# Kernel optimization log

Measured on AMD Instinct MI355X. Metric: run time of the kernel, lower is better.

## Reference

```python
import jax, jax.numpy as jnp
import numpy as np

EMBED_DIM = 1024
NUM_HEADS = 16
HEAD_DIM = EMBED_DIM // NUM_HEADS
SCALING = HEAD_DIM ** -0.5
TGT_LEN = 2048
BSZ = 2


def setup_inputs() -> dict:
    key = jax.random.key(0)
    ks = jax.random.split(key, 8)
    E = EMBED_DIM
    query = jax.random.normal(ks[0], (TGT_LEN, BSZ, E), dtype=jnp.float32)
    k_in = jax.random.normal(ks[1], (TGT_LEN, BSZ, E), dtype=jnp.float32)
    v_in = jax.random.normal(ks[2], (TGT_LEN, BSZ, E), dtype=jnp.float32)
    attn_mask = jnp.zeros((TGT_LEN, TGT_LEN), dtype=jnp.float32)
    key_padding_mask = jnp.zeros((1, TGT_LEN, TGT_LEN), dtype=jnp.int32)
    # torch.nn.Linear params: y = x @ W.T + b
    lim_qkv = 1.0 / np.sqrt(E)
    W_qkv = jax.random.uniform(ks[3], (3 * E, E), minval=-lim_qkv, maxval=lim_qkv, dtype=jnp.float32)
    b_qkv = jax.random.uniform(ks[4], (3 * E,), minval=-lim_qkv, maxval=lim_qkv, dtype=jnp.float32)
    W_out = jax.random.uniform(ks[5], (E, E), minval=-lim_qkv, maxval=lim_qkv, dtype=jnp.float32)
    b_out = jax.random.uniform(ks[6], (E,), minval=-lim_qkv, maxval=lim_qkv, dtype=jnp.float32)
    return {"query": query, "key": k_in, "value": v_in, "attn_mask": attn_mask,
            "key_padding_mask": key_padding_mask, "W_qkv": W_qkv, "b_qkv": b_qkv,
            "W_out": W_out, "b_out": b_out}


def reference(query, key, value, attn_mask, key_padding_mask, W_qkv, b_qkv, W_out, b_out):
    # NOTE: original module ignores `key`/`value` args (self-attn from query only).
    T, B, E = query.shape
    H, hd = NUM_HEADS, HEAD_DIM
    neg_inf = jnp.float32(-jnp.inf)
    qkv = query @ W_qkv.T + b_qkv                       # [T, B, 3E]
    qkv = jnp.transpose(qkv.reshape(T, B * H, 3 * hd), (1, 0, 2))  # [BH, T, 3hd]
    q, k, v = jnp.split(qkv, 3, axis=-1)                # each [BH, T, hd]
    aw = jnp.einsum('btd,bsd->bts', q, k) * SCALING     # [BH, T, T]
    # quirk of original: exact-zero scores become -inf
    aw = jnp.where(aw == 0, neg_inf, aw)
    am = jnp.where(attn_mask == 0, jnp.float32(0.0), attn_mask * jnp.float32(-10000.0))
    aw = aw + am
    aw = jnp.where(jnp.swapaxes(key_padding_mask, -2, -1) == 0, aw, neg_inf)
    aw = jax.nn.softmax(aw, axis=-1)
    # dropout p=0.0 -> identity
    out = aw @ v                                        # [BH, T, hd]
    # faithful to original: transpose(0,1) then reshape(bsz, tgt_len, E)
    out = jnp.swapaxes(out, 0, 1).reshape(B, T, E)      # [B, T, E]
    return out @ W_out.T + b_out
```

## Files before the change

### kernel.cpp

```cpp
#include <hip/hip_runtime.h>
#include <math.h>

#define TLEN 2048
#define EMB 1024
#define QKVD 3072
#define NROWS 4096
#define LOG2E 1.4426950408889634f

typedef unsigned short u16;
typedef unsigned int u32;
using frag_ab = __attribute__((ext_vector_type(8))) short;
using f32x4   = __attribute__((ext_vector_type(4))) float;

__device__ __forceinline__ u16 f2bf(float x) {
    u32 u = __builtin_bit_cast(u32, x);
    u = (u + 0x7FFFu + ((u >> 16) & 1u)) >> 16;
    return (u16)u;
}

__device__ __forceinline__ u32 cvt_pk_bf16(float lo, float hi) {
    u32 r;
    asm("v_cvt_pk_bf16_f32 %0, %1, %2" : "=v"(r) : "v"(lo), "v"(hi));
    return r;
}

__device__ __forceinline__ float exp2_hw(float x) {
    float r;
    asm("v_exp_f32 %0, %1" : "=v"(r) : "v"(x));
    return r;
}

#define GLL16(g, l) __builtin_amdgcn_global_load_lds(                         \
    (const __attribute__((address_space(1))) void*)(g),                       \
    (__attribute__((address_space(3))) void*)(l), 16, 0, 0)

__global__ __launch_bounds__(256)
void prep(const float* __restrict__ qa, const float* __restrict__ wqkv,
          const float* __restrict__ wout, u16* __restrict__ out,
          const float* __restrict__ am, const int* __restrict__ kpm,
          float* __restrict__ cm, int* __restrict__ flags)
{
    __shared__ int kt[64][65];
    __shared__ int s_any;
    const int tid = threadIdx.x;
    const int bid = blockIdx.x;
    if (bid < 4096) {
        int i = (bid * 256 + tid) * 8;
        const float* src;
        int off;
        if (i < 4194304)      { src = qa;   off = i; }
        else if (i < 7340032) { src = wqkv; off = i - 4194304; }
        else                  { src = wout; off = i - 7340032; }
        float4 x = *reinterpret_cast<const float4*>(src + off);
        float4 y = *reinterpret_cast<const float4*>(src + off + 4);
        union { u16 h[8]; uint4 v; } o;
        o.h[0] = f2bf(x.x); o.h[1] = f2bf(x.y); o.h[2] = f2bf(x.z); o.h[3] = f2bf(x.w);
        o.h[4] = f2bf(y.x); o.h[5] = f2bf(y.y); o.h[6] = f2bf(y.z); o.h[7] = f2bf(y.w);
        *reinterpret_cast<uint4*>(out + i) = o.v;
        return;
    }
    const int id2 = bid - 4096;
    const int s0 = (id2 & 31) * 64, t0 = (id2 >> 5) * 64;
    if (tid == 0) s_any = 0;
    #pragma unroll
    for (int u = 0; u < 4; ++u) {
        int idx = u * 256 + tid;
        int r  = idx >> 4;
        int cq = (idx & 15) * 4;
        int4 v = *reinterpret_cast<const int4*>(&kpm[(size_t)(s0 + r) * TLEN + t0 + cq]);
        kt[r][cq + 0] = v.x; kt[r][cq + 1] = v.y; kt[r][cq + 2] = v.z; kt[r][cq + 3] = v.w;
    }
    __syncthreads();
    float rbuf[4][4];
    int myany = 0;
    #pragma unroll
    for (int u = 0; u < 4; ++u) {
        int idx = u * 256 + tid;
        int r  = idx >> 4;
        int cq = (idx & 15) * 4;
        float4 a = *reinterpret_cast<const float4*>(&am[(size_t)(t0 + r) * TLEN + s0 + cq]);
        const float av[4] = {a.x, a.y, a.z, a.w};
        #pragma unroll
        for (int c = 0; c < 4; ++c) {
            float t = (av[c] == 0.0f) ? 0.0f : av[c] * -10000.0f;
            if (kt[cq + c][r] != 0) t = -INFINITY;
            rbuf[u][c] = t * LOG2E;
            myany |= (rbuf[u][c] != 0.0f);
        }
    }
    if (myany) s_any = 1;
    __syncthreads();
    if (s_any) {
        #pragma unroll
        for (int u = 0; u < 4; ++u) {
            int idx = u * 256 + tid;
            int r  = idx >> 4;
            int cq = (idx & 15) * 4;
            *reinterpret_cast<float4*>(&cm[(size_t)(t0 + r) * TLEN + s0 + cq]) =
                make_float4(rbuf[u][0], rbuf[u][1], rbuf[u][2], rbuf[u][3]);
        }
    }
    if (tid == 0) flags[id2] = s_any;
}

template <int OUT_MODE, int NF>
__global__ __launch_bounds__(256)
void gemm_nt_mfma(const u16* __restrict__ A, const u16* __restrict__ B,
                  const float* __restrict__ bias, void* __restrict__ Cp,
                  u16* __restrict__ Vg, int M, int N, int K)
{
    constexpr int BN = NF * 32;
    __shared__ u16 As[128 * 32];
    __shared__ u16 Bs[BN * 32];
    const int tid  = threadIdx.x;
    const int lane = tid & 63;
    const int w    = tid >> 6;
    const int wr   = w >> 1, wc = w & 1;

    const int nbx = N / BN;
    const int id  = blockIdx.x;
    const int lin = (id & 7) * ((int)gridDim.x >> 3) + (id >> 3);
    const int bm = (lin / nbx) * 128, bn = (lin % nbx) * BN;

    f32x4 acc[4][NF];
    #pragma unroll
    for (int i = 0; i < 4; ++i)
        #pragma unroll
        for (int j = 0; j < NF; ++j)
            acc[i][j] = (f32x4){0.f, 0.f, 0.f, 0.f};

    const int srow = tid >> 2;
    const int skel = (tid & 3) * 8;
    const u16* Ag = A + (size_t)(bm + srow) * K + skel;
    const u16* Bg = B + (size_t)(bn + srow % BN) * K + skel;
    u16* Asl = As + srow * 32 + skel;
    u16* Bsl = Bs + (srow % BN) * 32 + skel;

    const int fr = lane & 15;
    const int fk = (lane >> 4) * 8;

    for (int k0 = 0; k0 < K; k0 += 32) {
        GLL16(Ag + k0, Asl);
        GLL16(Ag + (size_t)64 * K + k0, Asl + 64 * 32);
        GLL16(Bg + k0, Bsl);
        if constexpr (NF == 4) GLL16(Bg + (size_t)64 * K + k0, Bsl + 64 * 32);
        __syncthreads();
        frag_ab af[4], bfr[NF];
        #pragma unroll
        for (int mf = 0; mf < 4; ++mf)
            af[mf] = *reinterpret_cast<const frag_ab*>(&As[(wr * 64 + mf * 16 + fr) * 32 + fk]);
        #pragma unroll
        for (int nf = 0; nf < NF; ++nf)
            bfr[nf] = *reinterpret_cast<const frag_ab*>(
                &Bs[(wc * (NF * 16) + nf * 16 + fr) * 32 + fk]);
        #pragma unroll
        for (int mf = 0; mf < 4; ++mf)
            #pragma unroll
            for (int nf = 0; nf < NF; ++nf)
                acc[mf][nf] = __builtin_amdgcn_mfma_f32_16x16x32_bf16(af[mf], bfr[nf], acc[mf][nf], 0, 0, 0);
        __syncthreads();
    }

    const int col0 = bn + wc * (NF * 16) + fr;
    const int row0 = bm + wr * 64 + (lane >> 4) * 4;
    #pragma unroll
    for (int nf = 0; nf < NF; ++nf) {
        const int col = col0 + nf * 16;
        const float bv = bias[col];
        if constexpr (OUT_MODE == 0) {
            #pragma unroll
            for (int mf = 0; mf < 4; ++mf)
                #pragma unroll
                for (int i = 0; i < 4; ++i)
                    ((float*)Cp)[(size_t)(row0 + mf * 16 + i) * N + col] = acc[mf][nf][i] + bv;
        } else {
            const u32 q6 = (u32)col >> 6;
            const u32 h = (q6 * 0xAAABu) >> 17;
            const int seg = col - (int)h * 192;
            if (seg < 128) {
                #pragma unroll
                for (int mf = 0; mf < 4; ++mf)
                    #pragma unroll
                    for (int i = 0; i < 4; ++i)
                        ((u16*)Cp)[(size_t)(row0 + mf * 16 + i) * N + col] =
                            f2bf(acc[mf][nf][i] + bv);
            } else {
                const int d = seg - 128;
                #pragma unroll
                for (int mf = 0; mf < 4; ++mf)
                    #pragma unroll
                    for (int i = 0; i < 4; ++i) {
                        const int row = row0 + mf * 16 + i;
                        Vg[(size_t)(((row & 1) * 16 + (int)h) * 64 + d) * TLEN + (row >> 1)] =
                            f2bf(acc[mf][nf][i] + bv);
                    }
            }
        }
    }
}

#define SM_KS 8192
#define SM_VT 24576

#define ATTN_STEP(CUR, NXT, IT, SIN, SOUT)                                    \
  {                                                                           \
                    \
    float vq[4][4];                                                           \
    _Pragma("unroll") for (int nf = 0; nf < 4; ++nf) {                        \
      _Pragma("unroll") for (int i = 0; i < 4; ++i) {                         \
        const float sv = SIN[nf][i];                                          \
        const float v = fmaf(SSCALE, sv, -24.0f);                             \
        vq[nf][i] = (sv == 0.0f) ? -INFINITY : v;                             \
      }                                                                       \
    }                                                                         \
    if (fmask & (1u << (IT))) {                                               \
      _Pragma("unroll") for (int nf = 0; nf < 4; ++nf) {                      \
        const float4 c4 = *reinterpret_cast<const float4*>(                   \
            &cm2[(size_t)rq * TLEN + (IT) * 64 + nf * 16 + 4 * fg]);          \
        vq[nf][0] += c4.x; vq[nf][1] += c4.y;                                 \
        vq[nf][2] += c4.z; vq[nf][3] += c4.w;                                 \
      }                                                                       \
    }                                                                         \
    float pv[4][4];                                                           \
    _Pragma("unroll") for (int nf = 0; nf < 4; ++nf) {                        \
      _Pragma("unroll") for (int i = 0; i < 4; ++i)                           \
        pv[nf][i] = exp2_hw(vq[nf][i]);                                       \
    }                                                                         \
    u32 pkA[4], pkB[4];                                                       \
    _Pragma("unroll") for (int nf = 0; nf < 4; ++nf) {                        \
      pkA[nf] = cvt_pk_bf16(pv[nf][0], pv[nf][1]);                            \
      pkB[nf] = cvt_pk_bf16(pv[nf][2], pv[nf][3]);                            \
    }                                                                         \
                      \
    __builtin_amdgcn_s_setprio(1);                                            \
    _Pragma("unroll") for (int ks = 0; ks < 2; ++ks) {                        \
      u32 d0 = pkA[2 * ks], d1 = pkB[2 * ks];                                 \
      u32 s0 = pkA[2 * ks + 1], s1 = pkB[2 * ks + 1];                         \
      asm("v_permlane32_swap_b32 %0, %1" : "+v"(d0), "+v"(s0));               \
      asm("v_permlane32_swap_b32 %0, %1" : "+v"(d1), "+v"(s1));               \
      const u32 sel0 = odd ? d0 : s0;                                         \
      const u32 sel1 = odd ? d1 : s1;                                         \
      const u32 r0_ = __builtin_amdgcn_ds_swizzle(sel0, 0x401F);              \
      const u32 r1_ = __builtin_amdgcn_ds_swizzle(sel1, 0x401F);              \
      union { u32 wq[4]; frag_ab f; } pau;                                    \
      pau.wq[0] = odd ? r0_ : d0;                                             \
      pau.wq[1] = odd ? r1_ : d1;                                             \
      pau.wq[2] = odd ? s0 : r0_;                                             \
      pau.wq[3] = odd ? s1 : r1_;                                             \
      _Pragma("unroll") for (int nf = 0; nf < 4; ++nf) {                      \
        frag_ab bv = *reinterpret_cast<const frag_ab*>(                       \
            smem + SM_VT + (CUR) * 8192 + nf * 2048 + (ks ? kb1 : kb0));      \
        oacc[nf] = __builtin_amdgcn_mfma_f32_16x16x32_bf16(pau.f, bv,         \
                                                           oacc[nf], 0, 0, 0); \
      }                                                                       \
      osum = __builtin_amdgcn_mfma_f32_16x16x32_bf16(pau.f, fones, osum,      \
                                                     0, 0, 0);                \
    }                                                                         \
    __builtin_amdgcn_s_setprio(0);                                            \
    asm volatile("s_waitcnt vmcnt(0)" ::: "memory");                          \
    __builtin_amdgcn_s_barrier();                                             \
          \
    {                                                                         \
      const int itn = ((IT) + 2 < 32) ? (IT) + 2 : 31;                        \
      GLL16(kbase + (size_t)((itn * 64 + srow) * 2 + b) * QKVD + gsrc,        \
            smem + SM_KS + (CUR) * 8192 + tid * 16);                          \
      GLL16(kbase + (size_t)((itn * 64 + 32 + srow) * 2 + b) * QKVD + gsrc,   \
            smem + SM_KS + (CUR) * 8192 + 4096 + tid * 16);                   \
      GLL16(vgbase + (size_t)srow * TLEN + itn * 64 + gsrc,                   \
            smem + SM_VT + (CUR) * 8192 + tid * 16);                          \
      GLL16(vgbase + (size_t)(srow + 32) * TLEN + itn * 64 + gsrc,            \
            smem + SM_VT + (CUR) * 8192 + 4096 + tid * 16);                   \
    }                                                                         \
     \
    _Pragma("unroll") for (int nf = 0; nf < 4; ++nf)                          \
      SOUT[nf] = (f32x4){0.f, 0.f, 0.f, 0.f};                                 \
    __builtin_amdgcn_s_setprio(1);                                            \
    _Pragma("unroll") for (int nf = 0; nf < 4; ++nf) {                        \
      _Pragma("unroll") for (int ks = 0; ks < 2; ++ks) {                      \
        frag_ab bk = *reinterpret_cast<const frag_ab*>(                       \
            smem + SM_KS + (NXT) * 8192 + nf * 2048 + (ks ? kb1 : kb0));      \
        SOUT[nf] = __builtin_amdgcn_mfma_f32_16x16x32_bf16(bk, aq[ks],        \
                                                           SOUT[nf], 0, 0, 0); \
      }                                                                       \
    }                                                                         \
    __builtin_amdgcn_s_setprio(0);                                            \
  }

__global__ __launch_bounds__(256, 4)
void attn_mfma(const u16* __restrict__ qkv, const float* __restrict__ cm2,
               const int* __restrict__ flags, const u16* __restrict__ Vg,
               u16* __restrict__ X2)
{
    __shared__ __attribute__((aligned(16))) char smem[40960];

    const int tid  = threadIdx.x;
    const int lane = tid & 63;
    const int w    = tid >> 6;

    const int id  = blockIdx.x;
    const int lin = (id & 7) * 128 + (id >> 3);
    const int bh  = lin >> 5;
    const int tt  = lin & 31;
    const int b = bh >> 4, h = bh & 15;
    const int t0 = tt * 64;

    const u16* qbase  = qkv + h * 192;
    const u16* kbase  = qkv + h * 192 + 64;
    const u16* vgbase = Vg + (size_t)bh * 64 * TLEN;

    const int srow = tid >> 3;
    const int sgl  = tid & 7;
    const int gsrc = ((sgl ^ (srow & 7)) & 7) * 8;
    const int fr = lane & 15;
    const int fg = lane >> 4;
    const bool odd = (lane & 16) != 0;
    const int rq = t0 + w * 16 + fr;

    const int kb0 = fr * 128 + (((fg) ^ (fr & 7)) & 7) * 16;
    const int kb1 = fr * 128 + (((4 + fg) ^ (fr & 7)) & 7) * 16;

    frag_ab fones;
    #pragma unroll
    for (int j = 0; j < 8; ++j) fones[j] = (short)0x3F80;

    const int* fl = flags + tt * 32;
    int fv = 0;
    if (lane < 32) fv = fl[lane];
    const u32 fmask = (u32)__ballot(fv != 0);

    GLL16(qbase + (size_t)((t0 + srow) * 2 + b) * QKVD + gsrc, smem + tid * 16);
    GLL16(qbase + (size_t)((t0 + 32 + srow) * 2 + b) * QKVD + gsrc, smem + 4096 + tid * 16);
    GLL16(kbase + (size_t)(srow * 2 + b) * QKVD + gsrc, smem + SM_KS + tid * 16);
    GLL16(kbase + (size_t)((32 + srow) * 2 + b) * QKVD + gsrc, smem + SM_KS + 4096 + tid * 16);
    GLL16(vgbase + (size_t)srow * TLEN + gsrc, smem + SM_VT + tid * 16);
    GLL16(vgbase + (size_t)(srow + 32) * TLEN + gsrc, smem + SM_VT + 4096 + tid * 16);
    __syncthreads();

    frag_ab aq[2];
    aq[0] = *reinterpret_cast<const frag_ab*>(smem + w * 2048 + kb0);
    aq[1] = *reinterpret_cast<const frag_ab*>(smem + w * 2048 + kb1);

    GLL16(kbase + (size_t)((64 + srow) * 2 + b) * QKVD + gsrc, smem + SM_KS + 8192 + tid * 16);
    GLL16(kbase + (size_t)((96 + srow) * 2 + b) * QKVD + gsrc, smem + SM_KS + 8192 + 4096 + tid * 16);
    GLL16(vgbase + (size_t)srow * TLEN + 64 + gsrc, smem + SM_VT + 8192 + tid * 16);
    GLL16(vgbase + (size_t)(srow + 32) * TLEN + 64 + gsrc, smem + SM_VT + 8192 + 4096 + tid * 16);

    f32x4 oacc[4];
    #pragma unroll
    for (int nf = 0; nf < 4; ++nf) oacc[nf] = (f32x4){0.f, 0.f, 0.f, 0.f};
    f32x4 osum = (f32x4){0.f, 0.f, 0.f, 0.f};
    f32x4 saccA[4], saccB[4];

    const float SSCALE = 0.125f * LOG2E;

    #pragma unroll
    for (int nf = 0; nf < 4; ++nf) saccA[nf] = (f32x4){0.f, 0.f, 0.f, 0.f};
    __builtin_amdgcn_s_setprio(1);
    #pragma unroll
    for (int nf = 0; nf < 4; ++nf) {
        #pragma unroll
        for (int ks = 0; ks < 2; ++ks) {
            frag_ab bk = *reinterpret_cast<const frag_ab*>(
                smem + SM_KS + nf * 2048 + (ks ? kb1 : kb0));
            saccA[nf] = __builtin_amdgcn_mfma_f32_16x16x32_bf16(bk, aq[ks],
                                                                saccA[nf], 0, 0, 0);
        }
    }
    __builtin_amdgcn_s_setprio(0);

    for (int it = 0; it < 32; it += 2) {
        ATTN_STEP(0, 1, it, saccA, saccB)
        ATTN_STEP(1, 0, it + 1, saccB, saccA)
    }

    #pragma unroll
    for (int i = 0; i < 4; ++i) {
        const int t = t0 + w * 16 + fg * 4 + i;
        const int rout = ((t >= 1024) ? 2048 : 0) + 2 * (t & 1023) + b;
        const float inv = 1.f / osum[i];
        #pragma unroll
        for (int nf = 0; nf < 4; ++nf)
            X2[(size_t)rout * EMB + h * 64 + nf * 16 + fr] = f2bf(oacc[nf][i] * inv);
    }
}

extern "C" void kernel_launch(void* const* d_in, const int* in_sizes, int n_in,
                              void* d_out, int out_size, void* d_ws, size_t ws_size,
                              hipStream_t stream)
{
    const float* query = (const float*)d_in[0];
    const float* am    = (const float*)d_in[3];
    const int*   kpm   = (const int*)d_in[4];
    const float* Wqkv  = (const float*)d_in[5];
    const float* bqkv  = (const float*)d_in[6];
    const float* Wout  = (const float*)d_in[7];
    const float* bout  = (const float*)d_in[8];
    float* out = (float*)d_out;

    char* ws = (char*)d_ws;
    u16*   qkv_bf  = (u16*)(ws);
    u16*   x2_bf   = (u16*)(ws + 25165824);
    float* cmask   = (float*)(ws + 33554432);
    u16*   q_bf    = (u16*)(ws + 50331648);
    u16*   wqkv_bf = (u16*)(ws + 58720256);
    u16*   wout_bf = (u16*)(ws + 65011712);
    int*   flags   = (int*)(ws + 67108864);
    u16*   v_tr    = (u16*)(ws + 67112960);

    prep<<<5120, 256, 0, stream>>>(query, Wqkv, Wout, q_bf, am, kpm, cmask, flags);

    gemm_nt_mfma<2, 4><<<768, 256, 0, stream>>>(q_bf, wqkv_bf, bqkv, qkv_bf,
                                                v_tr, NROWS, QKVD, EMB);
    attn_mfma<<<1024, 256, 0, stream>>>(qkv_bf, cmask, flags, v_tr, x2_bf);
    gemm_nt_mfma<0, 2><<<512, 256, 0, stream>>>(x2_bf, wout_bf, bout, out,
                                                nullptr, NROWS, EMB, EMB);
}
```

Before: 134.2 us.

## Share K/V tiles across 128 query rows and split the KV loop with a combine pass

Result: slower. 137.3 us (+2.3%).

```diff
diff --git a/kernel.cpp b/kernel.cpp
--- a/kernel.cpp
+++ b/kernel.cpp
@@ -16,6 +16,10 @@
     u32 u = __builtin_bit_cast(u32, x);
     u = (u + 0x7FFFu + ((u >> 16) & 1u)) >> 16;
     return (u16)u;
+}
+
+__device__ __forceinline__ float bf2f(u16 h) {
+    return __builtin_bit_cast(float, (u32)h << 16);
 }
 
 __device__ __forceinline__ u32 cvt_pk_bf16(float lo, float hi) {
@@ -199,10 +203,10 @@
     }
 }
 
-#define SM_KS 8192
-#define SM_VT 24576
-
-#define ATTN_STEP(CUR, NXT, IT, SIN, SOUT)                                    \
+#define SM_VT 16384
+#define SM_Q  32768
+
+#define ATTN_STEP(CUR, NXT, IT, SLIM, SIN, SOUT)                              \
   {                                                                           \
                     \
     float vq[4][4];                                                           \
@@ -261,24 +265,20 @@
     __builtin_amdgcn_s_barrier();                                             \
           \
     {                                                                         \
-      const int itn = ((IT) + 2 < 32) ? (IT) + 2 : 31;                        \
+      const int itn = ((IT) + 2 < (SLIM)) ? (IT) + 2 : (SLIM) - 1;            \
       GLL16(kbase + (size_t)((itn * 64 + srow) * 2 + b) * QKVD + gsrc,        \
-            smem + SM_KS + (CUR) * 8192 + tid * 16);                          \
-      GLL16(kbase + (size_t)((itn * 64 + 32 + srow) * 2 + b) * QKVD + gsrc,   \
-            smem + SM_KS + (CUR) * 8192 + 4096 + tid * 16);                   \
+            smem + (CUR) * 8192 + tid * 16);                                  \
       GLL16(vgbase + (size_t)srow * TLEN + itn * 64 + gsrc,                   \
             smem + SM_VT + (CUR) * 8192 + tid * 16);                          \
-      GLL16(vgbase + (size_t)(srow + 32) * TLEN + itn * 64 + gsrc,            \
-            smem + SM_VT + (CUR) * 8192 + 4096 + tid * 16);                   \
-    }                                                                         \
-     \
+    }                                                                         \
+                          \
     _Pragma("unroll") for (int nf = 0; nf < 4; ++nf)                          \
       SOUT[nf] = (f32x4){0.f, 0.f, 0.f, 0.f};                                 \
     __builtin_amdgcn_s_setprio(1);                                            \
     _Pragma("unroll") for (int nf = 0; nf < 4; ++nf) {                        \
       _Pragma("unroll") for (int ks = 0; ks < 2; ++ks) {                      \
         frag_ab bk = *reinterpret_cast<const frag_ab*>(                       \
-            smem + SM_KS + (NXT) * 8192 + nf * 2048 + (ks ? kb1 : kb0));      \
+            smem + (NXT) * 8192 + nf * 2048 + (ks ? kb1 : kb0));              \
         SOUT[nf] = __builtin_amdgcn_mfma_f32_16x16x32_bf16(bk, aq[ks],        \
                                                            SOUT[nf], 0, 0, 0); \
       }                                                                       \
@@ -286,23 +286,32 @@
     __builtin_amdgcn_s_setprio(0);                                            \
   }
 
-__global__ __launch_bounds__(256, 4)
+template <int NHALF>
+__global__ __launch_bounds__(512, 6)
 void attn_mfma(const u16* __restrict__ qkv, const float* __restrict__ cm2,
                const int* __restrict__ flags, const u16* __restrict__ Vg,
-               u16* __restrict__ X2)
+               u16* __restrict__ X2, u16* __restrict__ opart,
+               float* __restrict__ lpart)
 {
-    __shared__ __attribute__((aligned(16))) char smem[40960];
+    __shared__ __attribute__((aligned(16))) char smem[49152];
 
     const int tid  = threadIdx.x;
     const int lane = tid & 63;
     const int w    = tid >> 6;
 
     const int id  = blockIdx.x;
-    const int lin = (id & 7) * 128 + (id >> 3);
-    const int bh  = lin >> 5;
-    const int tt  = lin & 31;
+    const int cpx = 64 * NHALF;
+    const int lin = (id & 7) * cpx + (id >> 3);
+    int bh, tt, half;
+    if constexpr (NHALF == 2) {
+        bh = lin >> 5;  tt = (lin & 31) >> 1;  half = lin & 1;
+    } else {
+        bh = lin >> 4;  tt = lin & 15;         half = 0;
+    }
     const int b = bh >> 4, h = bh & 15;
-    const int t0 = tt * 64;
+    const int t0 = tt * 128;
+    const int sb = half * (32 / NHALF);
+    const int slim = sb + 32 / NHALF;
 
     const u16* qbase  = qkv + h * 192;
     const u16* kbase  = qkv + h * 192 + 64;
@@ -323,27 +332,25 @@
     #pragma unroll
     for (int j = 0; j < 8; ++j) fones[j] = (short)0x3F80;
 
-    const int* fl = flags + tt * 32;
+    const int* fl = flags + ((t0 >> 6) + (w >> 2)) * 32;
     int fv = 0;
     if (lane < 32) fv = fl[lane];
     const u32 fmask = (u32)__ballot(fv != 0);
 
-    GLL16(qbase + (size_t)((t0 + srow) * 2 + b) * QKVD + gsrc, smem + tid * 16);
-    GLL16(qbase + (size_t)((t0 + 32 + srow) * 2 + b) * QKVD + gsrc, smem + 4096 + tid * 16);
-    GLL16(kbase + (size_t)(srow * 2 + b) * QKVD + gsrc, smem + SM_KS + tid * 16);
-    GLL16(kbase + (size_t)((32 + srow) * 2 + b) * QKVD + gsrc, smem + SM_KS + 4096 + tid * 16);
-    GLL16(vgbase + (size_t)srow * TLEN + gsrc, smem + SM_VT + tid * 16);
-    GLL16(vgbase + (size_t)(srow + 32) * TLEN + gsrc, smem + SM_VT + 4096 + tid * 16);
+    GLL16(qbase + (size_t)((t0 + srow) * 2 + b) * QKVD + gsrc, smem + SM_Q + tid * 16);
+    GLL16(qbase + (size_t)((t0 + 64 + srow) * 2 + b) * QKVD + gsrc, smem + SM_Q + 8192 + tid * 16);
+    GLL16(kbase + (size_t)((sb * 64 + srow) * 2 + b) * QKVD + gsrc, smem + tid * 16);
+    GLL16(vgbase + (size_t)srow * TLEN + sb * 64 + gsrc, smem + SM_VT + tid * 16);
     __syncthreads();
 
     frag_ab aq[2];
-    aq[0] = *reinterpret_cast<const frag_ab*>(smem + w * 2048 + kb0);
-    aq[1] = *reinterpret_cast<const frag_ab*>(smem + w * 2048 + kb1);
-
-    GLL16(kbase + (size_t)((64 + srow) * 2 + b) * QKVD + gsrc, smem + SM_KS + 8192 + tid * 16);
-    GLL16(kbase + (size_t)((96 + srow) * 2 + b) * QKVD + gsrc, smem + SM_KS + 8192 + 4096 + tid * 16);
-    GLL16(vgbase + (size_t)srow * TLEN + 64 + gsrc, smem + SM_VT + 8192 + tid * 16);
-    GLL16(vgbase + (size_t)(srow + 32) * TLEN + 64 + gsrc, smem + SM_VT + 8192 + 4096 + tid * 16);
+    aq[0] = *reinterpret_cast<const frag_ab*>(smem + SM_Q + w * 2048 + kb0);
+    aq[1] = *reinterpret_cast<const frag_ab*>(smem + SM_Q + w * 2048 + kb1);
+
+    GLL16(kbase + (size_t)(((sb + 1) * 64 + srow) * 2 + b) * QKVD + gsrc,
+          smem + 8192 + tid * 16);
+    GLL16(vgbase + (size_t)srow * TLEN + (sb + 1) * 64 + gsrc,
+          smem + SM_VT + 8192 + tid * 16);
 
     f32x4 oacc[4];
     #pragma unroll
@@ -361,26 +368,74 @@
         #pragma unroll
         for (int ks = 0; ks < 2; ++ks) {
             frag_ab bk = *reinterpret_cast<const frag_ab*>(
-                smem + SM_KS + nf * 2048 + (ks ? kb1 : kb0));
+                smem + nf * 2048 + (ks ? kb1 : kb0));
             saccA[nf] = __builtin_amdgcn_mfma_f32_16x16x32_bf16(bk, aq[ks],
                                                                 saccA[nf], 0, 0, 0);
         }
     }
     __builtin_amdgcn_s_setprio(0);
 
-    for (int it = 0; it < 32; it += 2) {
-        ATTN_STEP(0, 1, it, saccA, saccB)
-        ATTN_STEP(1, 0, it + 1, saccB, saccA)
-    }
-
-    #pragma unroll
-    for (int i = 0; i < 4; ++i) {
-        const int t = t0 + w * 16 + fg * 4 + i;
-        const int rout = ((t >= 1024) ? 2048 : 0) + 2 * (t & 1023) + b;
-        const float inv = 1.f / osum[i];
-        #pragma unroll
-        for (int nf = 0; nf < 4; ++nf)
-            X2[(size_t)rout * EMB + h * 64 + nf * 16 + fr] = f2bf(oacc[nf][i] * inv);
+    for (int it2 = sb; it2 < slim; it2 += 2) {
+        ATTN_STEP(0, 1, it2, slim, saccA, saccB)
+        ATTN_STEP(1, 0, it2 + 1, slim, saccB, saccA)
+    }
+
+    if constexpr (NHALF == 2) {
+        const int pidx = (bh * 16 + tt) * 2 + half;
+        u16* ob = opart + (size_t)pidx * 8192;
+        #pragma unroll
+        for (int i = 0; i < 4; ++i) {
+            const int row = w * 16 + fg * 4 + i;
+            #pragma unroll
+            for (int nf = 0; nf < 4; ++nf)
+                ob[row * 64 + nf * 16 + fr] = f2bf(oacc[nf][i]);
+            if (fr == 0) lpart[pidx * 128 + row] = osum[i];
+        }
+    } else {
+        #pragma unroll
+        for (int i = 0; i < 4; ++i) {
+            const int t = t0 + w * 16 + fg * 4 + i;
+            const int rout = ((t >= 1024) ? 2048 : 0) + 2 * (t & 1023) + b;
+            const float inv = 1.f / osum[i];
+            #pragma unroll
+            for (int nf = 0; nf < 4; ++nf)
+                X2[(size_t)rout * EMB + h * 64 + nf * 16 + fr] = f2bf(oacc[nf][i] * inv);
+        }
+    }
+}
+
+__global__ __launch_bounds__(256)
+void combine(const u16* __restrict__ opart, const float* __restrict__ lpart,
+             u16* __restrict__ X2)
+{
+    const int b2 = blockIdx.x;
+    const int bh = b2 >> 4, tt = b2 & 15;
+    const int b = bh >> 4, h = bh & 15;
+    const int tid = threadIdx.x;
+    const int r = tid >> 1;
+    const int dbase = (tid & 1) * 32;
+    const int p0 = (bh * 16 + tt) * 2;
+    const u16* o0 = opart + (size_t)p0 * 8192 + r * 64 + dbase;
+    const u16* o1 = o0 + 8192;
+    const float inv = 1.f / (lpart[p0 * 128 + r] + lpart[(p0 + 1) * 128 + r]);
+    const int t = tt * 128 + r;
+    const int rout = ((t >= 1024) ? 2048 : 0) + 2 * (t & 1023) + b;
+    u16* dst = X2 + (size_t)rout * EMB + h * 64 + dbase;
+    #pragma unroll
+    for (int j = 0; j < 4; ++j) {
+        uint4 a = *reinterpret_cast<const uint4*>(o0 + j * 8);
+        uint4 c = *reinterpret_cast<const uint4*>(o1 + j * 8);
+        const u32 aw[4] = {a.x, a.y, a.z, a.w};
+        const u32 cw[4] = {c.x, c.y, c.z, c.w};
+        union { u16 hh[8]; uint4 v; } o;
+        #pragma unroll
+        for (int k = 0; k < 4; ++k) {
+            const float lo = (bf2f((u16)aw[k]) + bf2f((u16)cw[k])) * inv;
+            const float hi = (bf2f((u16)(aw[k] >> 16)) + bf2f((u16)(cw[k] >> 16))) * inv;
+            o.hh[2 * k]     = f2bf(lo);
+            o.hh[2 * k + 1] = f2bf(hi);
+        }
+        *reinterpret_cast<uint4*>(dst + j * 8) = o.v;
     }
 }
 
@@ -406,12 +461,23 @@
     u16*   wout_bf = (u16*)(ws + 65011712);
     int*   flags   = (int*)(ws + 67108864);
     u16*   v_tr    = (u16*)(ws + 67112960);
+    u16*   opart   = (u16*)(ws + 75501568);
+    float* lpart   = (float*)(ws + 92278784);
+
+    const bool split = ws_size >= 92803072u;
 
     prep<<<5120, 256, 0, stream>>>(query, Wqkv, Wout, q_bf, am, kpm, cmask, flags);
 
     gemm_nt_mfma<2, 4><<<768, 256, 0, stream>>>(q_bf, wqkv_bf, bqkv, qkv_bf,
                                                 v_tr, NROWS, QKVD, EMB);
-    attn_mfma<<<1024, 256, 0, stream>>>(qkv_bf, cmask, flags, v_tr, x2_bf);
+    if (split) {
+        attn_mfma<2><<<1024, 512, 0, stream>>>(qkv_bf, cmask, flags, v_tr,
+                                               nullptr, opart, lpart);
+        combine<<<512, 256, 0, stream>>>(opart, lpart, x2_bf);
+    } else {
+        attn_mfma<1><<<512, 512, 0, stream>>>(qkv_bf, cmask, flags, v_tr,
+                                              x2_bf, nullptr, nullptr);
+    }
     gemm_nt_mfma<0, 2><<<512, 256, 0, stream>>>(x2_bf, wout_bf, bout, out,
                                                 nullptr, NROWS, EMB, EMB);
 }
```

## Process 128 query rows per attention block with 8 waves sharing K/V tiles

Applied to the files above, without the earlier changes.

Result: faster. 130.1 us (median of 2 runs) (-3.1%).

```diff
diff --git a/kernel.cpp b/kernel.cpp
--- a/kernel.cpp
+++ b/kernel.cpp
@@ -199,12 +199,10 @@
     }
 }
 
-#define SM_KS 8192
-#define SM_VT 24576
+#define SM_VT 16384
 
 #define ATTN_STEP(CUR, NXT, IT, SIN, SOUT)                                    \
   {                                                                           \
-                    \
     float vq[4][4];                                                           \
     _Pragma("unroll") for (int nf = 0; nf < 4; ++nf) {                        \
       _Pragma("unroll") for (int i = 0; i < 4; ++i) {                         \
@@ -231,7 +229,6 @@
       pkA[nf] = cvt_pk_bf16(pv[nf][0], pv[nf][1]);                            \
       pkB[nf] = cvt_pk_bf16(pv[nf][2], pv[nf][3]);                            \
     }                                                                         \
-                      \
     __builtin_amdgcn_s_setprio(1);                                            \
     _Pragma("unroll") for (int ks = 0; ks < 2; ++ks) {                        \
       u32 d0 = pkA[2 * ks], d1 = pkB[2 * ks];                                 \
@@ -259,26 +256,20 @@
     __builtin_amdgcn_s_setprio(0);                                            \
     asm volatile("s_waitcnt vmcnt(0)" ::: "memory");                          \
     __builtin_amdgcn_s_barrier();                                             \
-          \
     {                                                                         \
       const int itn = ((IT) + 2 < 32) ? (IT) + 2 : 31;                        \
       GLL16(kbase + (size_t)((itn * 64 + srow) * 2 + b) * QKVD + gsrc,        \
-            smem + SM_KS + (CUR) * 8192 + tid * 16);                          \
-      GLL16(kbase + (size_t)((itn * 64 + 32 + srow) * 2 + b) * QKVD + gsrc,   \
-            smem + SM_KS + (CUR) * 8192 + 4096 + tid * 16);                   \
+            smem + (CUR) * 8192 + tid * 16);                                  \
       GLL16(vgbase + (size_t)srow * TLEN + itn * 64 + gsrc,                   \
             smem + SM_VT + (CUR) * 8192 + tid * 16);                          \
-      GLL16(vgbase + (size_t)(srow + 32) * TLEN + itn * 64 + gsrc,            \
-            smem + SM_VT + (CUR) * 8192 + 4096 + tid * 16);                   \
-    }                                                                         \
-     \
+    }                                                                         \
     _Pragma("unroll") for (int nf = 0; nf < 4; ++nf)                          \
       SOUT[nf] = (f32x4){0.f, 0.f, 0.f, 0.f};                                 \
     __builtin_amdgcn_s_setprio(1);                                            \
     _Pragma("unroll") for (int nf = 0; nf < 4; ++nf) {                        \
       _Pragma("unroll") for (int ks = 0; ks < 2; ++ks) {                      \
         frag_ab bk = *reinterpret_cast<const frag_ab*>(                       \
-            smem + SM_KS + (NXT) * 8192 + nf * 2048 + (ks ? kb1 : kb0));      \
+            smem + (NXT) * 8192 + nf * 2048 + (ks ? kb1 : kb0));              \
         SOUT[nf] = __builtin_amdgcn_mfma_f32_16x16x32_bf16(bk, aq[ks],        \
                                                            SOUT[nf], 0, 0, 0); \
       }                                                                       \
@@ -286,25 +277,24 @@
     __builtin_amdgcn_s_setprio(0);                                            \
   }
 
-__global__ __launch_bounds__(256, 4)
+__global__ __launch_bounds__(512, 6)
 void attn_mfma(const u16* __restrict__ qkv, const float* __restrict__ cm2,
                const int* __restrict__ flags, const u16* __restrict__ Vg,
                u16* __restrict__ X2)
 {
-    __shared__ __attribute__((aligned(16))) char smem[40960];
+    __shared__ __attribute__((aligned(16))) char smem[32768];
 
     const int tid  = threadIdx.x;
     const int lane = tid & 63;
     const int w    = tid >> 6;
 
     const int id  = blockIdx.x;
-    const int lin = (id & 7) * 128 + (id >> 3);
-    const int bh  = lin >> 5;
-    const int tt  = lin & 31;
+    const int lin = (id & 7) * 64 + (id >> 3);
+    const int bh  = lin >> 4;
+    const int tt  = lin & 15;
     const int b = bh >> 4, h = bh & 15;
-    const int t0 = tt * 64;
-
-    const u16* qbase  = qkv + h * 192;
+    const int t0 = tt * 128;
+
     const u16* kbase  = qkv + h * 192 + 64;
     const u16* vgbase = Vg + (size_t)bh * 64 * TLEN;
 
@@ -323,27 +313,23 @@
     #pragma unroll
     for (int j = 0; j < 8; ++j) fones[j] = (short)0x3F80;
 
-    const int* fl = flags + tt * 32;
+    const int* fl = flags + ((t0 >> 6) + (w >> 2)) * 32;
     int fv = 0;
     if (lane < 32) fv = fl[lane];
     const u32 fmask = (u32)__ballot(fv != 0);
 
-    GLL16(qbase + (size_t)((t0 + srow) * 2 + b) * QKVD + gsrc, smem + tid * 16);
-    GLL16(qbase + (size_t)((t0 + 32 + srow) * 2 + b) * QKVD + gsrc, smem + 4096 + tid * 16);
-    GLL16(kbase + (size_t)(srow * 2 + b) * QKVD + gsrc, smem + SM_KS + tid * 16);
-    GLL16(kbase + (size_t)((32 + srow) * 2 + b) * QKVD + gsrc, smem + SM_KS + 4096 + tid * 16);
+    frag_ab aq[2];
+    {
+        const u16* qrow = qkv + (size_t)(rq * 2 + b) * QKVD + h * 192;
+        aq[0] = *reinterpret_cast<const frag_ab*>(qrow + fg * 8);
+        aq[1] = *reinterpret_cast<const frag_ab*>(qrow + (4 + fg) * 8);
+    }
+
+    GLL16(kbase + (size_t)(srow * 2 + b) * QKVD + gsrc, smem + tid * 16);
     GLL16(vgbase + (size_t)srow * TLEN + gsrc, smem + SM_VT + tid * 16);
-    GLL16(vgbase + (size_t)(srow + 32) * TLEN + gsrc, smem + SM_VT + 4096 + tid * 16);
+    GLL16(kbase + (size_t)((64 + srow) * 2 + b) * QKVD + gsrc, smem + 8192 + tid * 16);
+    GLL16(vgbase + (size_t)srow * TLEN + 64 + gsrc, smem + SM_VT + 8192 + tid * 16);
     __syncthreads();
-
-    frag_ab aq[2];
-    aq[0] = *reinterpret_cast<const frag_ab*>(smem + w * 2048 + kb0);
-    aq[1] = *reinterpret_cast<const frag_ab*>(smem + w * 2048 + kb1);
-
-    GLL16(kbase + (size_t)((64 + srow) * 2 + b) * QKVD + gsrc, smem + SM_KS + 8192 + tid * 16);
-    GLL16(kbase + (size_t)((96 + srow) * 2 + b) * QKVD + gsrc, smem + SM_KS + 8192 + 4096 + tid * 16);
-    GLL16(vgbase + (size_t)srow * TLEN + 64 + gsrc, smem + SM_VT + 8192 + tid * 16);
-    GLL16(vgbase + (size_t)(srow + 32) * TLEN + 64 + gsrc, smem + SM_VT + 8192 + 4096 + tid * 16);
 
     f32x4 oacc[4];
     #pragma unroll
@@ -361,16 +347,16 @@
         #pragma unroll
         for (int ks = 0; ks < 2; ++ks) {
             frag_ab bk = *reinterpret_cast<const frag_ab*>(
-                smem + SM_KS + nf * 2048 + (ks ? kb1 : kb0));
+                smem + nf * 2048 + (ks ? kb1 : kb0));
             saccA[nf] = __builtin_amdgcn_mfma_f32_16x16x32_bf16(bk, aq[ks],
                                                                 saccA[nf], 0, 0, 0);
         }
     }
     __builtin_amdgcn_s_setprio(0);
 
-    for (int it = 0; it < 32; it += 2) {
-        ATTN_STEP(0, 1, it, saccA, saccB)
-        ATTN_STEP(1, 0, it + 1, saccB, saccA)
+    for (int it2 = 0; it2 < 32; it2 += 2) {
+        ATTN_STEP(0, 1, it2, saccA, saccB)
+        ATTN_STEP(1, 0, it2 + 1, saccB, saccA)
     }
 
     #pragma unroll
@@ -411,7 +397,7 @@
 
     gemm_nt_mfma<2, 4><<<768, 256, 0, stream>>>(q_bf, wqkv_bf, bqkv, qkv_bf,
                                                 v_tr, NROWS, QKVD, EMB);
-    attn_mfma<<<1024, 256, 0, stream>>>(qkv_bf, cmask, flags, v_tr, x2_bf);
+    attn_mfma<<<512, 512, 0, stream>>>(qkv_bf, cmask, flags, v_tr, x2_bf);
     gemm_nt_mfma<0, 2><<<512, 256, 0, stream>>>(x2_bf, wout_bf, bout, out,
                                                 nullptr, NROWS, EMB, EMB);
 }
```
